# Optimization experiments

Measured on AMD Instinct MI355X. Metric: run time of the kernel, lower is better.

The kernel has to match this reference:

```python
import jax, jax.numpy as jnp
import numpy as np

D_K = 64  # per-head dim, used as softmax scale (matches __init__ d_k)

def setup_inputs() -> dict:
    key = jax.random.key(0)
    kq, kk, kv, km = jax.random.split(key, 4)
    B, H, S, D = 2, 16, 2048, D_K
    q = jax.random.normal(kq, (B, H, S, D), dtype=jnp.float32)
    k = jax.random.normal(kk, (B, H, S, D), dtype=jnp.float32)
    v = jax.random.normal(kv, (B, H, S, D), dtype=jnp.float32)
    mask = jax.random.randint(km, (B, 1, S, S), 0, 2).astype(jnp.bool_)
    return {"q": q, "k": k, "v": v, "mask": mask}

def reference(q, k, v, mask):
    # attn = (q / sqrt(d_k)) @ k^T  -> [B,H,S,S]
    scale = 1.0 / jnp.sqrt(jnp.float32(D_K))
    attn = jnp.einsum("bhqd,bhkd->bhqk", q * scale, k)
    # faithful to torch masked_fill(mask, -1e-09) -- note tiny value, not -1e9
    attn = jnp.where(mask, jnp.float32(-1e-9), attn)
    weights = jax.nn.softmax(attn, axis=-1)  # dropout p=0.0 -> identity
    output = jnp.einsum("bhqk,bhkd->bhqd", weights, v)
    return (output, weights)
```

## Files before the change

kernel.cpp:

```cpp
#include <hip/hip_runtime.h>
#include <hip/hip_bf16.h>


namespace {

constexpr int kS = 2048;
constexpr int kD = 64;
constexpr int kBH = 32;
constexpr int kTQW = 16;
constexpr int kNW = 4;
constexpr int kTQB = kTQW * kNW;
constexpr int kChunk = 64;
constexpr int kNC = kS / kChunk;
constexpr int kNB = kBH * (kS / kTQB);
constexpr size_t kWOff = (size_t)kBH * kS * kD;

typedef __attribute__((ext_vector_type(8))) short bf16x8;
typedef __attribute__((ext_vector_type(4))) short bf16x4;
typedef __attribute__((ext_vector_type(4))) float f32x4;

__device__ inline short f2bf(float f) {
  union { float f; unsigned u; } x; x.f = f;
  return (short)((x.u + 0x7fffu + ((x.u >> 16) & 1u)) >> 16);
}

__device__ inline unsigned pk2bf(float a, float b) {
  return (unsigned)(unsigned short)f2bf(a) | ((unsigned)(unsigned short)f2bf(b) << 16);
}

__device__ inline bf16x8 cvt8(float4 a, float4 b, float scale) {
  bf16x8 f;
  f[0] = f2bf(a.x * scale); f[1] = f2bf(a.y * scale);
  f[2] = f2bf(a.z * scale); f[3] = f2bf(a.w * scale);
  f[4] = f2bf(b.x * scale); f[5] = f2bf(b.y * scale);
  f[6] = f2bf(b.z * scale); f[7] = f2bf(b.w * scale);
  return f;
}

__device__ inline f32x4 mfma32(bf16x8 a, bf16x8 b, f32x4 c) {
  return __builtin_amdgcn_mfma_f32_16x16x32_bf16(a, b, c, 0, 0, 0);
}

__device__ inline f32x4 mfma16(bf16x4 a, bf16x4 b, f32x4 c) {
#if __has_builtin(__builtin_amdgcn_mfma_f32_16x16x16bf16_1k)
  return __builtin_amdgcn_mfma_f32_16x16x16bf16_1k(a, b, c, 0, 0, 0);
#elif __has_builtin(__builtin_amdgcn_mfma_f32_16x16x16_bf16)
  return __builtin_amdgcn_mfma_f32_16x16x16_bf16(a, b, c, 0, 0, 0);
#else
  f32x4 d = c;
  asm volatile("v_mfma_f32_16x16x16_bf16 %0, %1, %2, %0" : "+v"(d) : "v"(a), "v"(b));
  return d;
#endif
}

__device__ inline void block_sync_lds() {
  asm volatile("s_waitcnt lgkmcnt(0)" ::: "memory");
  __builtin_amdgcn_s_barrier();
  asm volatile("" ::: "memory");
}

__global__ __launch_bounds__(256, 4) void attn_fused(
    const float* __restrict__ qg, const float* __restrict__ kg,
    const float* __restrict__ vg, const unsigned int* __restrict__ mg,
    float* __restrict__ outg) {
  __shared__ __align__(16) short SH[18944];
  short (*K0)[72] = (short(*)[72])(SH);
  short (*K1)[72] = (short(*)[72])(SH + 4608);
  short (*V0)[72] = (short(*)[72])(SH + 9216);
  short (*V1)[72] = (short(*)[72])(SH + 13824);
  unsigned short* Msk0 = (unsigned short*)(SH + 18432);
  unsigned short* Msk1 = (unsigned short*)(SH + 18688);

  const int tid  = threadIdx.x;
  const int wv   = tid >> 6;
  const int lane = tid & 63;
  const int l15  = lane & 15;
  const int quad = lane >> 4;

  const int bid  = blockIdx.x;
  const int work = ((bid & 7) << 7) | (bid >> 3);
  const int qt   = work & 31;
  const int bh   = work >> 5;
  const int b    = bh >> 4;
  const int q0b  = qt * kTQB;

  int allW32 = 1, allI32 = 1, allBF = 1;
#pragma unroll
  for (int i = 0; i < 64; ++i) {
    const unsigned u = mg[i];
    const unsigned lo = u & 0xFFFFu, hi = u >> 16;
    allW32 &= (int)(u == 0u || u == 0x3F800000u);
    allI32 &= (int)(u == 0u || u == 1u);
    allBF  &= (int)((lo == 0u || lo == 0x3F80u) && (hi == 0u || hi == 0x3F80u));
  }
  int msz;
  if (allI32)      msz = 4;
  else if (allW32) msz = 4;
  else if (allBF)  msz = 2;
  else             msz = 1;
  const unsigned char* mB = (const unsigned char*)mg + (size_t)b * kS * kS * msz;

  const float* qbase = qg + (size_t)bh * kS * kD;
  const float* kbase = kg + (size_t)bh * kS * kD;
  const float* vbase = vg + (size_t)bh * kS * kD;
  float* obase = outg + (size_t)bh * kS * kD;
  float* wbase = outg + kWOff + (size_t)bh * kS * kS;

  const int qrow = q0b + wv * kTQW + l15;
  const int mrow = wv * kTQW + l15;

  bf16x8 aq[2];
#pragma unroll
  for (int dh = 0; dh < 2; ++dh) {
    const float* p = qbase + (size_t)qrow * kD + dh * 32 + quad * 8;
    aq[dh] = cvt8(*(const float4*)p, *(const float4*)(p + 4), 0.125f);
  }

  const int si  = tid >> 2;
  const int sj  = (tid & 3) << 4;
  const int sjw = tid & 3;
  const int vd  = (tid & 7) << 3;
  const int vk  = (tid >> 3) << 1;
  float4 rk[4], rv[4];
  uint4 mrg[4];

  auto k_issue = [&](int c) {
    const float* p = kbase + (size_t)(c * kChunk + si) * kD + sj;
    rk[0] = *(const float4*)p;       rk[1] = *(const float4*)(p + 4);
    rk[2] = *(const float4*)(p + 8); rk[3] = *(const float4*)(p + 12);
  };
  auto k_write = [&](short (*Kdst)[72]) {
    *(bf16x8*)&Kdst[si][sj]     = cvt8(rk[0], rk[1], 1.0f);
    *(bf16x8*)&Kdst[si][sj + 8] = cvt8(rk[2], rk[3], 1.0f);
  };

  auto v_issue = [&](int c) {
    const float* p = vbase + (size_t)(c * kChunk + vk) * kD + vd;
    rv[0] = *(const float4*)p;        rv[1] = *(const float4*)(p + 4);
    rv[2] = *(const float4*)(p + kD); rv[3] = *(const float4*)(p + kD + 4);
  };
  auto v_write = [&](short (*Vdst)[72]) {
    const float* lo = (const float*)&rv[0];
    const float* hi = (const float*)&rv[2];
#pragma unroll
    for (int d = 0; d < 8; ++d) {
      const int dd = vd + d;
      const int ps = (vk >> 1) ^ (((dd >> 3) & 7) << 2);
      *(unsigned*)&Vdst[dd][2 * ps] = pk2bf(lo[d], hi[d]);
    }
  };

  auto m_issue = [&](int c) {
    const size_t base = (size_t)(q0b + si) * kS + (size_t)(c * kChunk) + sjw * 16;
    if (msz == 4) {
      const uint4* p = (const uint4*)((const unsigned*)mB + base);
      mrg[0] = p[0]; mrg[1] = p[1]; mrg[2] = p[2]; mrg[3] = p[3];
    } else if (msz == 2) {
      const uint4* p = (const uint4*)((const unsigned short*)mB + base);
      mrg[0] = p[0]; mrg[1] = p[1];
    } else {
      mrg[0] = *(const uint4*)(mB + base);
    }
  };
  auto m_write = [&](unsigned short* Mdst) {
    unsigned bits = 0;
    if (msz == 4) {
#pragma unroll
      for (int g = 0; g < 4; ++g) {
        const uint4 e = mrg[g];
        bits |= (e.x ? 1u : 0u) << (4 * g + 0);
        bits |= (e.y ? 1u : 0u) << (4 * g + 1);
        bits |= (e.z ? 1u : 0u) << (4 * g + 2);
        bits |= (e.w ? 1u : 0u) << (4 * g + 3);
      }
    } else if (msz == 2) {
#pragma unroll
      for (int g = 0; g < 2; ++g) {
        const uint4 e = mrg[g];
        bits |= ((e.x & 0xFFFFu) ? 1u : 0u) << (8 * g + 0);
        bits |= ((e.x >> 16)     ? 1u : 0u) << (8 * g + 1);
        bits |= ((e.y & 0xFFFFu) ? 1u : 0u) << (8 * g + 2);
        bits |= ((e.y >> 16)     ? 1u : 0u) << (8 * g + 3);
        bits |= ((e.z & 0xFFFFu) ? 1u : 0u) << (8 * g + 4);
        bits |= ((e.z >> 16)     ? 1u : 0u) << (8 * g + 5);
        bits |= ((e.w & 0xFFFFu) ? 1u : 0u) << (8 * g + 6);
        bits |= ((e.w >> 16)     ? 1u : 0u) << (8 * g + 7);
      }
    } else {
      const uint4 e = mrg[0];
#pragma unroll
      for (int by = 0; by < 4; ++by) {
        bits |= (((e.x >> (8 * by)) & 0xFFu) ? 1u : 0u) << (0 + by);
        bits |= (((e.y >> (8 * by)) & 0xFFu) ? 1u : 0u) << (4 + by);
        bits |= (((e.z >> (8 * by)) & 0xFFu) ? 1u : 0u) << (8 + by);
        bits |= (((e.w >> (8 * by)) & 0xFFu) ? 1u : 0u) << (12 + by);
      }
    }
    Mdst[si * 4 + sjw] = (unsigned short)bits;
  };

  float lsum = 0.f;
  k_issue(0); m_issue(0);
  k_write(K0); m_write(Msk0);
  k_issue(1); m_issue(1);
  block_sync_lds();
  for (int c = 0; c < kNC; ++c) {
    if (c + 1 < kNC) { k_write((c & 1) ? K0 : K1); m_write((c & 1) ? Msk0 : Msk1); }
    if (c + 2 < kNC) { k_issue(c + 2); m_issue(c + 2); }
    short (*K)[72] = (c & 1) ? K1 : K0;
    const unsigned short* M = (c & 1) ? Msk1 : Msk0;
    const unsigned long long mbits = *(const unsigned long long*)&M[mrow * 4];
    __builtin_amdgcn_s_setprio(1);
#pragma unroll
    for (int t = 0; t < 4; ++t) {
      bf16x8 f0 = *(const bf16x8*)&K[t * 16 + l15][quad * 8];
      bf16x8 f1 = *(const bf16x8*)&K[t * 16 + l15][32 + quad * 8];
      f32x4 acc = {0.f, 0.f, 0.f, 0.f};
      acc = mfma32(f0, aq[0], acc);
      acc = mfma32(f1, aq[1], acc);
      const unsigned nib = (unsigned)(mbits >> (16 * t + 4 * quad)) & 0xFu;
#pragma unroll
      for (int r = 0; r < 4; ++r) {
        const float e = __expf(acc[r]);
        lsum += (nib & (1u << r)) ? 1.0f : e;
      }
    }
    __builtin_amdgcn_s_setprio(0);
    block_sync_lds();
  }

  lsum += __shfl_xor(lsum, 16);
  lsum += __shfl_xor(lsum, 32);
  const float inv = 1.0f / lsum;

  f32x4 acco[4];
#pragma unroll
  for (int d = 0; d < 4; ++d) acco[d] = (f32x4){0.f, 0.f, 0.f, 0.f};

  k_issue(0); v_issue(0); m_issue(0);
  k_write(K0); v_write(V0); m_write(Msk0);
  k_issue(1); v_issue(1); m_issue(1);
  block_sync_lds();
  float* const wrow = wbase + (size_t)qrow * kS;
  for (int c = 0; c < kNC; ++c) {
    if (c + 1 < kNC) {
      k_write((c & 1) ? K0 : K1); v_write((c & 1) ? V0 : V1);
      m_write((c & 1) ? Msk0 : Msk1);
    }
    if (c + 2 < kNC) { k_issue(c + 2); v_issue(c + 2); m_issue(c + 2); }
    short (*K)[72] = (c & 1) ? K1 : K0;
    short (*V)[72] = (c & 1) ? V1 : V0;
    const unsigned short* M = (c & 1) ? Msk1 : Msk0;
    const unsigned long long mbits = *(const unsigned long long*)&M[mrow * 4];
    __builtin_amdgcn_s_setprio(1);
#pragma unroll
    for (int t = 0; t < 4; ++t) {
      bf16x8 f0 = *(const bf16x8*)&K[t * 16 + l15][quad * 8];
      bf16x8 f1 = *(const bf16x8*)&K[t * 16 + l15][32 + quad * 8];
      f32x4 acc = {0.f, 0.f, 0.f, 0.f};
      acc = mfma32(f0, aq[0], acc);
      acc = mfma32(f1, aq[1], acc);
      const unsigned nib = (unsigned)(mbits >> (16 * t + 4 * quad)) & 0xFu;
      const float w0 = ((nib & 1u) ? 1.0f : __expf(acc[0])) * inv;
      const float w1 = ((nib & 2u) ? 1.0f : __expf(acc[1])) * inv;
      const float w2 = ((nib & 4u) ? 1.0f : __expf(acc[2])) * inv;
      const float w3 = ((nib & 8u) ? 1.0f : __expf(acc[3])) * inv;
      *(f32x4*)(wrow + c * kChunk + t * 16 + quad * 4) = (f32x4){w0, w1, w2, w3};
      const bf16x4 wfrag = {f2bf(w0), f2bf(w1), f2bf(w2), f2bf(w3)};
#pragma unroll
      for (int dt = 0; dt < 4; ++dt) {
        const int dd = dt * 16 + l15;
        const int pp = (8 * t + 2 * quad) ^ (((dd >> 3) & 7) << 2);
        const bf16x4 vfrag = *(const bf16x4*)&V[dd][2 * pp];
        acco[dt] = mfma16(vfrag, wfrag, acco[dt]);
      }
    }
    __builtin_amdgcn_s_setprio(0);
    block_sync_lds();
  }

#pragma unroll
  for (int dt = 0; dt < 4; ++dt)
    *(f32x4*)(obase + (size_t)qrow * kD + dt * 16 + quad * 4) = acco[dt];
}

}

extern "C" void kernel_launch(void* const* d_in, const int* in_sizes, int n_in,
                              void* d_out, int out_size, void* d_ws, size_t ws_size,
                              hipStream_t stream) {
  const float* q = (const float*)d_in[0];
  const float* k = (const float*)d_in[1];
  const float* v = (const float*)d_in[2];
  const unsigned int* mask = (const unsigned int*)d_in[3];
  float* out = (float*)d_out;
  attn_fused<<<dim3(kNB), dim3(256), 0, stream>>>(q, k, v, mask, out);
}
```

Measured before the change: 811.5 us.

## Split softmax denominator pass into separate split-K kernel with scratch in weights output

The single fused kernel ran a row-sum pass and then a weights/PV pass in sequence within each block. The row-sum pass now runs as its own kernel, split across two key halves to double the grid, at higher occupancy (launch bounds 8) and with smaller LDS. The partial sums are parked in the first two elements of each weights row and read back by the PV kernel, which overwrites them. This adds a second launch and relies on the second kernel reading those slots before it overwrites them, but it exposes more parallelism for the first pass.

```diff
diff --git a/kernel.cpp b/kernel.cpp
--- a/kernel.cpp
+++ b/kernel.cpp
@@ -1,5 +1,4 @@
 #include <hip/hip_runtime.h>
-#include <hip/hip_bf16.h>
 
 
 namespace {
@@ -11,8 +10,10 @@
 constexpr int kNW = 4;
 constexpr int kTQB = kTQW * kNW;
 constexpr int kChunk = 64;
-constexpr int kNC = kS / kChunk;
-constexpr int kNB = kBH * (kS / kTQB);
+constexpr int kNCB = kS / kChunk;
+constexpr int kNCA = kNCB / 2;
+constexpr int kNBB = kBH * (kS / kTQB);
+constexpr int kNBA = kNBB * 2;
 constexpr size_t kWOff = (size_t)kBH * kS * kD;
 
 typedef __attribute__((ext_vector_type(8))) short bf16x8;
@@ -28,12 +29,12 @@
   return (unsigned)(unsigned short)f2bf(a) | ((unsigned)(unsigned short)f2bf(b) << 16);
 }
 
-__device__ inline bf16x8 cvt8(float4 a, float4 b, float scale) {
+__device__ inline bf16x8 cvt8(float4 a, float4 b, float s) {
   bf16x8 f;
-  f[0] = f2bf(a.x * scale); f[1] = f2bf(a.y * scale);
-  f[2] = f2bf(a.z * scale); f[3] = f2bf(a.w * scale);
-  f[4] = f2bf(b.x * scale); f[5] = f2bf(b.y * scale);
-  f[6] = f2bf(b.z * scale); f[7] = f2bf(b.w * scale);
+  f[0] = f2bf(a.x * s); f[1] = f2bf(a.y * s);
+  f[2] = f2bf(a.z * s); f[3] = f2bf(a.w * s);
+  f[4] = f2bf(b.x * s); f[5] = f2bf(b.y * s);
+  f[6] = f2bf(b.z * s); f[7] = f2bf(b.w * s);
   return f;
 }
 
@@ -59,9 +60,164 @@
   asm volatile("" ::: "memory");
 }
 
-__global__ __launch_bounds__(256, 4) void attn_fused(
+__device__ inline int detect_msz(const unsigned* __restrict__ mg) {
+  int allW32 = 1, allI32 = 1, allBF = 1;
+#pragma unroll
+  for (int i = 0; i < 64; ++i) {
+    const unsigned u = mg[i];
+    const unsigned lo = u & 0xFFFFu, hi = u >> 16;
+    allW32 &= (int)(u == 0u || u == 0x3F800000u);
+    allI32 &= (int)(u == 0u || u == 1u);
+    allBF  &= (int)((lo == 0u || lo == 0x3F80u) && (hi == 0u || hi == 0x3F80u));
+  }
+  if (allI32) return 4;
+  if (allW32) return 4;
+  if (allBF)  return 2;
+  return 1;
+}
+
+__global__ __launch_bounds__(256, 8) void attn_lsum(
     const float* __restrict__ qg, const float* __restrict__ kg,
-    const float* __restrict__ vg, const unsigned int* __restrict__ mg,
+    const unsigned* __restrict__ mg, float* __restrict__ outg) {
+  __shared__ __align__(16) short SH[9728];
+  short (*K0)[72] = (short(*)[72])(SH);
+  short (*K1)[72] = (short(*)[72])(SH + 4608);
+  unsigned short* Msk0 = (unsigned short*)(SH + 9216);
+  unsigned short* Msk1 = (unsigned short*)(SH + 9472);
+
+  const int tid  = threadIdx.x;
+  const int wv   = tid >> 6;
+  const int lane = tid & 63;
+  const int l15  = lane & 15;
+  const int quad = lane >> 4;
+
+  const int bid  = blockIdx.x;
+  const int work = ((bid & 7) << 8) | (bid >> 3);
+  const int half = work & 1;
+  const int qt   = (work >> 1) & 31;
+  const int bh   = work >> 6;
+  const int b    = bh >> 4;
+  const int q0b  = qt * kTQB;
+  const int kOff = half * (kS / 2);
+
+  const int msz = detect_msz(mg);
+  const unsigned char* mB = (const unsigned char*)mg + (size_t)b * kS * kS * msz;
+  const float* qbase = qg + (size_t)bh * kS * kD;
+  const float* kbase = kg + (size_t)bh * kS * kD;
+  float* wbase = outg + kWOff + (size_t)bh * kS * kS;
+
+  const int qrow = q0b + wv * kTQW + l15;
+  const int mrow = wv * kTQW + l15;
+
+  bf16x8 aq[2];
+#pragma unroll
+  for (int dh = 0; dh < 2; ++dh) {
+    const float* p = qbase + (size_t)qrow * kD + dh * 32 + quad * 8;
+    aq[dh] = cvt8(*(const float4*)p, *(const float4*)(p + 4), 0.125f);
+  }
+
+  const int si  = tid >> 2;
+  const int sj  = (tid & 3) << 4;
+  const int sjw = tid & 3;
+  float4 rk[4];
+  uint4 mrg[4];
+
+  auto k_issue = [&](int c) {
+    const float* p = kbase + (size_t)(kOff + c * kChunk + si) * kD + sj;
+    rk[0] = *(const float4*)p;       rk[1] = *(const float4*)(p + 4);
+    rk[2] = *(const float4*)(p + 8); rk[3] = *(const float4*)(p + 12);
+  };
+  auto k_write = [&](short (*Kdst)[72]) {
+    *(bf16x8*)&Kdst[si][sj]     = cvt8(rk[0], rk[1], 1.0f);
+    *(bf16x8*)&Kdst[si][sj + 8] = cvt8(rk[2], rk[3], 1.0f);
+  };
+  auto m_issue = [&](int c) {
+    const size_t base = (size_t)(q0b + si) * kS + (size_t)(kOff + c * kChunk) + sjw * 16;
+    if (msz == 4) {
+      const uint4* p = (const uint4*)((const unsigned*)mB + base);
+      mrg[0] = p[0]; mrg[1] = p[1]; mrg[2] = p[2]; mrg[3] = p[3];
+    } else if (msz == 2) {
+      const uint4* p = (const uint4*)((const unsigned short*)mB + base);
+      mrg[0] = p[0]; mrg[1] = p[1];
+    } else {
+      mrg[0] = *(const uint4*)(mB + base);
+    }
+  };
+  auto m_write = [&](unsigned short* Mdst) {
+    unsigned bits = 0;
+    if (msz == 4) {
+#pragma unroll
+      for (int g = 0; g < 4; ++g) {
+        const uint4 e = mrg[g];
+        bits |= (e.x ? 1u : 0u) << (4 * g + 0);
+        bits |= (e.y ? 1u : 0u) << (4 * g + 1);
+        bits |= (e.z ? 1u : 0u) << (4 * g + 2);
+        bits |= (e.w ? 1u : 0u) << (4 * g + 3);
+      }
+    } else if (msz == 2) {
+#pragma unroll
+      for (int g = 0; g < 2; ++g) {
+        const uint4 e = mrg[g];
+        bits |= ((e.x & 0xFFFFu) ? 1u : 0u) << (8 * g + 0);
+        bits |= ((e.x >> 16)     ? 1u : 0u) << (8 * g + 1);
+        bits |= ((e.y & 0xFFFFu) ? 1u : 0u) << (8 * g + 2);
+        bits |= ((e.y >> 16)     ? 1u : 0u) << (8 * g + 3);
+        bits |= ((e.z & 0xFFFFu) ? 1u : 0u) << (8 * g + 4);
+        bits |= ((e.z >> 16)     ? 1u : 0u) << (8 * g + 5);
+        bits |= ((e.w & 0xFFFFu) ? 1u : 0u) << (8 * g + 6);
+        bits |= ((e.w >> 16)     ? 1u : 0u) << (8 * g + 7);
+      }
+    } else {
+      const uint4 e = mrg[0];
+#pragma unroll
+      for (int by = 0; by < 4; ++by) {
+        bits |= (((e.x >> (8 * by)) & 0xFFu) ? 1u : 0u) << (0 + by);
+        bits |= (((e.y >> (8 * by)) & 0xFFu) ? 1u : 0u) << (4 + by);
+        bits |= (((e.z >> (8 * by)) & 0xFFu) ? 1u : 0u) << (8 + by);
+        bits |= (((e.w >> (8 * by)) & 0xFFu) ? 1u : 0u) << (12 + by);
+      }
+    }
+    Mdst[si * 4 + sjw] = (unsigned short)bits;
+  };
+
+  float lsum = 0.f;
+  k_issue(0); m_issue(0);
+  k_write(K0); m_write(Msk0);
+  k_issue(1); m_issue(1);
+  block_sync_lds();
+  for (int c = 0; c < kNCA; ++c) {
+    if (c + 1 < kNCA) { k_write((c & 1) ? K0 : K1); m_write((c & 1) ? Msk0 : Msk1); }
+    if (c + 2 < kNCA) { k_issue(c + 2); m_issue(c + 2); }
+    short (*K)[72] = (c & 1) ? K1 : K0;
+    const unsigned short* M = (c & 1) ? Msk1 : Msk0;
+    const unsigned long long mbits = *(const unsigned long long*)&M[mrow * 4];
+    __builtin_amdgcn_s_setprio(1);
+#pragma unroll
+    for (int t = 0; t < 4; ++t) {
+      bf16x8 f0 = *(const bf16x8*)&K[t * 16 + l15][quad * 8];
+      bf16x8 f1 = *(const bf16x8*)&K[t * 16 + l15][32 + quad * 8];
+      f32x4 acc = {0.f, 0.f, 0.f, 0.f};
+      acc = mfma32(f0, aq[0], acc);
+      acc = mfma32(f1, aq[1], acc);
+      const unsigned nib = (unsigned)(mbits >> (16 * t + 4 * quad)) & 0xFu;
+#pragma unroll
+      for (int r = 0; r < 4; ++r) {
+        const float e = __expf(acc[r]);
+        lsum += (nib & (1u << r)) ? 1.0f : e;
+      }
+    }
+    __builtin_amdgcn_s_setprio(0);
+    block_sync_lds();
+  }
+
+  lsum += __shfl_xor(lsum, 16);
+  lsum += __shfl_xor(lsum, 32);
+  if (lane < 16) wbase[(size_t)qrow * kS + half] = lsum;
+}
+
+__global__ __launch_bounds__(256, 4) void attn_pv(
+    const float* __restrict__ qg, const float* __restrict__ kg,
+    const float* __restrict__ vg, const unsigned* __restrict__ mg,
     float* __restrict__ outg) {
   __shared__ __align__(16) short SH[18944];
   short (*K0)[72] = (short(*)[72])(SH);
@@ -84,22 +240,8 @@
   const int b    = bh >> 4;
   const int q0b  = qt * kTQB;
 
-  int allW32 = 1, allI32 = 1, allBF = 1;
-#pragma unroll
-  for (int i = 0; i < 64; ++i) {
-    const unsigned u = mg[i];
-    const unsigned lo = u & 0xFFFFu, hi = u >> 16;
-    allW32 &= (int)(u == 0u || u == 0x3F800000u);
-    allI32 &= (int)(u == 0u || u == 1u);
-    allBF  &= (int)((lo == 0u || lo == 0x3F80u) && (hi == 0u || hi == 0x3F80u));
-  }
-  int msz;
-  if (allI32)      msz = 4;
-  else if (allW32) msz = 4;
-  else if (allBF)  msz = 2;
-  else             msz = 1;
+  const int msz = detect_msz(mg);
   const unsigned char* mB = (const unsigned char*)mg + (size_t)b * kS * kS * msz;
-
   const float* qbase = qg + (size_t)bh * kS * kD;
   const float* kbase = kg + (size_t)bh * kS * kD;
   const float* vbase = vg + (size_t)bh * kS * kD;
@@ -108,6 +250,11 @@
 
   const int qrow = q0b + wv * kTQW + l15;
   const int mrow = wv * kTQW + l15;
+  float* const wrow = wbase + (size_t)qrow * kS;
+
+  const float pa0 = wrow[0];
+  const float pa1 = wrow[1];
+  const float inv = 1.0f / (pa0 + pa1);
 
   bf16x8 aq[2];
 #pragma unroll
@@ -133,7 +280,6 @@
     *(bf16x8*)&Kdst[si][sj]     = cvt8(rk[0], rk[1], 1.0f);
     *(bf16x8*)&Kdst[si][sj + 8] = cvt8(rk[2], rk[3], 1.0f);
   };
-
   auto v_issue = [&](int c) {
     const float* p = vbase + (size_t)(c * kChunk + vk) * kD + vd;
     rv[0] = *(const float4*)p;        rv[1] = *(const float4*)(p + 4);
@@ -149,7 +295,6 @@
       *(unsigned*)&Vdst[dd][2 * ps] = pk2bf(lo[d], hi[d]);
     }
   };
-
   auto m_issue = [&](int c) {
     const size_t base = (size_t)(q0b + si) * kS + (size_t)(c * kChunk) + sjw * 16;
     if (msz == 4) {
@@ -199,40 +344,6 @@
     Mdst[si * 4 + sjw] = (unsigned short)bits;
   };
 
-  float lsum = 0.f;
-  k_issue(0); m_issue(0);
-  k_write(K0); m_write(Msk0);
-  k_issue(1); m_issue(1);
-  block_sync_lds();
-  for (int c = 0; c < kNC; ++c) {
-    if (c + 1 < kNC) { k_write((c & 1) ? K0 : K1); m_write((c & 1) ? Msk0 : Msk1); }
-    if (c + 2 < kNC) { k_issue(c + 2); m_issue(c + 2); }
-    short (*K)[72] = (c & 1) ? K1 : K0;
-    const unsigned short* M = (c & 1) ? Msk1 : Msk0;
-    const unsigned long long mbits = *(const unsigned long long*)&M[mrow * 4];
-    __builtin_amdgcn_s_setprio(1);
-#pragma unroll
-    for (int t = 0; t < 4; ++t) {
-      bf16x8 f0 = *(const bf16x8*)&K[t * 16 + l15][quad * 8];
-      bf16x8 f1 = *(const bf16x8*)&K[t * 16 + l15][32 + quad * 8];
-      f32x4 acc = {0.f, 0.f, 0.f, 0.f};
-      acc = mfma32(f0, aq[0], acc);
-      acc = mfma32(f1, aq[1], acc);
-      const unsigned nib = (unsigned)(mbits >> (16 * t + 4 * quad)) & 0xFu;
-#pragma unroll
-      for (int r = 0; r < 4; ++r) {
-        const float e = __expf(acc[r]);
-        lsum += (nib & (1u << r)) ? 1.0f : e;
-      }
-    }
-    __builtin_amdgcn_s_setprio(0);
-    block_sync_lds();
-  }
-
-  lsum += __shfl_xor(lsum, 16);
-  lsum += __shfl_xor(lsum, 32);
-  const float inv = 1.0f / lsum;
-
   f32x4 acco[4];
 #pragma unroll
   for (int d = 0; d < 4; ++d) acco[d] = (f32x4){0.f, 0.f, 0.f, 0.f};
@@ -241,13 +352,12 @@
   k_write(K0); v_write(V0); m_write(Msk0);
   k_issue(1); v_issue(1); m_issue(1);
   block_sync_lds();
-  float* const wrow = wbase + (size_t)qrow * kS;
-  for (int c = 0; c < kNC; ++c) {
-    if (c + 1 < kNC) {
+  for (int c = 0; c < kNCB; ++c) {
+    if (c + 1 < kNCB) {
       k_write((c & 1) ? K0 : K1); v_write((c & 1) ? V0 : V1);
       m_write((c & 1) ? Msk0 : Msk1);
     }
-    if (c + 2 < kNC) { k_issue(c + 2); v_issue(c + 2); m_issue(c + 2); }
+    if (c + 2 < kNCB) { k_issue(c + 2); v_issue(c + 2); m_issue(c + 2); }
     short (*K)[72] = (c & 1) ? K1 : K0;
     short (*V)[72] = (c & 1) ? V1 : V0;
     const unsigned short* M = (c & 1) ? Msk1 : Msk0;
@@ -292,7 +402,8 @@
   const float* q = (const float*)d_in[0];
   const float* k = (const float*)d_in[1];
   const float* v = (const float*)d_in[2];
-  const unsigned int* mask = (const unsigned int*)d_in[3];
+  const unsigned* mask = (const unsigned*)d_in[3];
   float* out = (float*)d_out;
-  attn_fused<<<dim3(kNB), dim3(256), 0, stream>>>(q, k, v, mask, out);
-}
+  attn_lsum<<<dim3(kNBA), dim3(256), 0, stream>>>(q, k, mask, out);
+  attn_pv<<<dim3(kNBB), dim3(256), 0, stream>>>(q, k, v, mask, out);
+}
```

Result: slower. 1.049 ms (+29.3%).
